# Performance work log

Measured on AMD Instinct MI355X. Metric: run time of the kernel, lower is better.

The kernel has to match this reference:

```python
import jax, jax.numpy as jnp
import numpy as np

# Regularized layout for the per-batch masked attention:
#   batch_size B=8, each batch has NF=2048 'fill' points followed by NK=4096 'keep' points.
B, NF, NK = 8, 2048, 4096
C_IN, C_KQ, C_OUT = 256, 64, 256


def setup_inputs() -> dict:
    key = jax.random.key(0)
    ks = jax.random.split(key, 7)
    N = B * (NF + NK)
    features = jax.random.normal(ks[0], (N, C_IN), dtype=jnp.float32)
    # keep flag: 0 for fill points, 1 for keep points, per batch (fill-first layout)
    flag = jnp.tile(jnp.concatenate([jnp.zeros(NF, jnp.int32), jnp.ones(NK, jnp.int32)]), B)
    s = 1.0 / np.sqrt(C_IN)
    Wq = jax.random.normal(ks[1], (C_KQ, C_IN), jnp.float32) * s
    bq = jnp.zeros((C_KQ,), jnp.float32)
    Wk = jax.random.normal(ks[2], (C_KQ, C_IN), jnp.float32) * s
    bk = jnp.zeros((C_KQ,), jnp.float32)
    Wv = jax.random.normal(ks[3], (C_OUT, C_IN), jnp.float32) * s
    bv = jnp.zeros((C_OUT,), jnp.float32)
    return {"features": features, "keep_flag": flag,
            "Wq": Wq, "bq": bq, "Wk": Wk, "bk": bk, "Wv": Wv, "bv": bv}


def reference(features, keep_flag, Wq, bq, Wk, bk, Wv, bv):
    # features: [N, C_IN]; keep_flag encodes the fill/keep split, which in this
    # regular layout is: first NF rows of each batch are fill, remaining NK are keep.
    del keep_flag  # structure is encoded in the layout (fill-first per batch)
    f = features.reshape(B, NF + NK, C_IN)
    fill = f[:, :NF]             # [B, NF, C_IN]
    keep = f[:, NF:]             # [B, NK, C_IN]
    q = fill @ Wq.T + bq         # [B, NF, C_KQ]
    k = keep @ Wk.T + bk         # [B, NK, C_KQ]
    v = keep @ Wv.T + bv         # [B, NK, C_OUT]
    ratio = np.sqrt(C_KQ).astype(np.float32)
    scores = jnp.einsum('bfd,bkd->bfk', q, k) / ratio   # [B, NF, NK]
    attn = jax.nn.softmax(scores, axis=-1)
    out_fill = jnp.einsum('bfk,bkc->bfc', attn, v)      # [B, NF, C_OUT]
    # keep rows pass through unchanged (only fill rows are overwritten)
    out = jnp.concatenate([out_fill, keep], axis=1)
    return out.reshape(B * (NF + NK), C_OUT)
```

## Files before the change

### kernel.cpp

```cpp
#include <hip/hip_runtime.h>
#include <hip/hip_bf16.h>

#define BATCHES 8
#define NFILL 2048
#define NKEEP 4096
#define SEQLEN 6144
#define CIN 256
#define CKQ 64
#define COUT 256

#define KSC 0.18033688011112042f
#define KOFF -11.541560327111707f

typedef __bf16 bf16_t;
typedef float f32x4 __attribute__((ext_vector_type(4)));
typedef bf16_t bf16x8 __attribute__((ext_vector_type(8)));

__device__ inline void cvt8_store(bf16_t* dst, float4 a, float4 b) {
  bf16x8 v;
  v[0] = (bf16_t)a.x; v[1] = (bf16_t)a.y; v[2] = (bf16_t)a.z; v[3] = (bf16_t)a.w;
  v[4] = (bf16_t)b.x; v[5] = (bf16_t)b.y; v[6] = (bf16_t)b.z; v[7] = (bf16_t)b.w;
  *(bf16x8*)dst = v;
}

__global__ __launch_bounds__(256, 2) void gemm_qkv(
    const float* __restrict__ feat, const float* __restrict__ Wq,
    const float* __restrict__ bq, const float* __restrict__ Wk,
    const float* __restrict__ bk, const float* __restrict__ Wv,
    const float* __restrict__ bv, bf16_t* __restrict__ Qw,
    bf16_t* __restrict__ Kw, bf16_t* __restrict__ Vw,
    float* __restrict__ outp) {
  __shared__ bf16_t Xs[64][264];
  __shared__ bf16_t Ws[64][264];

  const int bid = blockIdx.x;
  const bool isQ = bid >= 512;
  const int mb = isQ ? bid - 512 : bid;

  const int t = threadIdx.x;
  const int lane = t & 63;
  const int wv = t >> 6;
  const int l16 = lane & 15;
  const int quad = lane >> 4;

  const int lr = t >> 2;
  const int koff = (t & 3) << 4;

  const int mrow = mb * 64 + lr;
  const int rpb_shift = isQ ? 11 : 12;
  const int batch = mrow >> rpb_shift;
  const int ridx = mrow & ((1 << rpb_shift) - 1);
  const int row_off = isQ ? 0 : NFILL;
  const long grow = (long)(batch * SEQLEN + row_off + ridx);
  const float* xptr = feat + grow * CIN;
  float4* orow = (float4*)(outp + grow * COUT);

  float4 wr[4][4];
  {
    const float* wrow0 = (isQ ? Wq : Wk) + (long)lr * CIN + koff;
#pragma unroll
    for (int j = 0; j < 4; j++)
#pragma unroll
      for (int s = 0; s < 4; s++)
        wr[j][s] = *(const float4*)(wrow0 + j * 64 + s * 4);
  }

#pragma unroll
  for (int j = 0; j < 4; j++) {
    const int c = koff + j * 64;
    float4 x0 = *(const float4*)(xptr + c);
    float4 x1 = *(const float4*)(xptr + c + 4);
    float4 x2 = *(const float4*)(xptr + c + 8);
    float4 x3 = *(const float4*)(xptr + c + 12);
    cvt8_store(&Xs[lr][c], x0, x1);
    cvt8_store(&Xs[lr][c + 8], x2, x3);
    if (!isQ) {
      orow[(c >> 2) + 0] = x0;
      orow[(c >> 2) + 1] = x1;
      orow[(c >> 2) + 2] = x2;
      orow[(c >> 2) + 3] = x3;
    }
  }
  __syncthreads();

  const int NT = isQ ? 1 : 5;
  const int vb = (mb * 64) >> 12;
  const int key0base = (mb * 64) & 4095;

  for (int nt = 0; nt < NT; nt++) {
#pragma unroll
    for (int j = 0; j < 4; j++) {
      cvt8_store(&Ws[lr][j * 64 + koff], wr[j][0], wr[j][1]);
      cvt8_store(&Ws[lr][j * 64 + koff + 8], wr[j][2], wr[j][3]);
    }
    if (nt + 1 < NT) {
      const float* wrow = Wv + ((long)(nt * 64) + lr) * CIN + koff;
#pragma unroll
      for (int j = 0; j < 4; j++)
#pragma unroll
        for (int s = 0; s < 4; s++)
          wr[j][s] = *(const float4*)(wrow + j * 64 + s * 4);
    }
    asm volatile("s_waitcnt lgkmcnt(0)\n\ts_barrier" ::: "memory");

    f32x4 acc[4];
#pragma unroll
    for (int nb = 0; nb < 4; nb++) acc[nb] = f32x4{0.f, 0.f, 0.f, 0.f};

    if (nt == 0) {
#pragma unroll
      for (int k0 = 0; k0 < CIN; k0 += 64) {
#pragma unroll
        for (int ks = 0; ks < 2; ks++) {
          bf16x8 afrag = *(const bf16x8*)&Xs[wv * 16 + l16][k0 + ks * 32 + quad * 8];
#pragma unroll
          for (int nb = 0; nb < 4; nb++) {
            bf16x8 bfrag = *(const bf16x8*)&Ws[nb * 16 + l16][k0 + ks * 32 + quad * 8];
            acc[nb] = __builtin_amdgcn_mfma_f32_16x16x32_bf16(afrag, bfrag, acc[nb], 0, 0, 0);
          }
        }
      }
      const float* bias = isQ ? bq : bk;
      bf16_t* op = isQ ? Qw : Kw;
#pragma unroll
      for (int nb = 0; nb < 4; nb++) {
        const int n = nb * 16 + l16;
        const float bb = bias[n];
#pragma unroll
        for (int r = 0; r < 4; r++) {
          const int m = mb * 64 + wv * 16 + quad * 4 + r;
          op[(long)m * CKQ + n] = (bf16_t)(acc[nb][r] + bb);
        }
      }
    } else {
#pragma unroll
      for (int k0 = 0; k0 < CIN; k0 += 64) {
#pragma unroll
        for (int ks = 0; ks < 2; ks++) {
          bf16x8 xfrag = *(const bf16x8*)&Xs[wv * 16 + l16][k0 + ks * 32 + quad * 8];
#pragma unroll
          for (int nb = 0; nb < 4; nb++) {
            bf16x8 wfrag = *(const bf16x8*)&Ws[nb * 16 + l16][k0 + ks * 32 + quad * 8];
            acc[nb] = __builtin_amdgcn_mfma_f32_16x16x32_bf16(wfrag, xfrag, acc[nb], 0, 0, 0);
          }
        }
      }
      const int n0 = (nt - 1) * 64;
#pragma unroll
      for (int nb = 0; nb < 4; nb++) {
        f32x4 bbv = *(const f32x4*)&bv[n0 + nb * 16 + quad * 4];
        bf16_t* vdst = Vw +
                       ((long)(vb * COUT + n0 + nb * 16 + quad * 4)) * NKEEP +
                       key0base + wv * 16 + l16;
#pragma unroll
        for (int r = 0; r < 4; r++)
          vdst[(long)r * NKEEP] = (bf16_t)(acc[nb][r] + bbv[r]);
      }
    }

    if (nt + 1 < NT)
      asm volatile("s_waitcnt lgkmcnt(0)\n\ts_barrier" ::: "memory");
  }
}

__global__ __launch_bounds__(256) void attn_kernel(
    const bf16_t* __restrict__ Q, const bf16_t* __restrict__ K,
    const bf16_t* __restrict__ Vt, float* __restrict__ outp) {
  __shared__ bf16_t Ks[2][64][72];
  __shared__ bf16_t Ps[64][72];
  __shared__ float Lsh[64];

  const int qt = blockIdx.x;
  const int b = blockIdx.y;
  const int t = threadIdx.x;
  const int lane = t & 63;
  const int wv = t >> 6;
  const int l16 = lane & 15;
  const int quad = lane >> 4;

  const int krow = t >> 2;
  const int kcol = (t & 3) << 4;

  const bf16_t* kbase = K + (long)b * NKEEP * CKQ;
  const int c0 = wv * 64;
  const bf16_t* vlane =
      Vt + ((long)(b * COUT + c0 + l16)) * NKEEP + quad * 8;

  bf16x8 qfrag[2];
  {
    const bf16_t* qrow = Q + ((long)(b * NFILL + qt * 64 + wv * 16 + l16)) * CKQ;
#pragma unroll
    for (int ks = 0; ks < 2; ks++)
      qfrag[ks] = *(const bf16x8*)(qrow + ks * 32 + quad * 8);
  }

  f32x4 oacc[4][4];
#pragma unroll
  for (int m = 0; m < 4; m++)
#pragma unroll
    for (int ct = 0; ct < 4; ct++) oacc[m][ct] = f32x4{0.f, 0.f, 0.f, 0.f};
  float rsum[4] = {0.f, 0.f, 0.f, 0.f};

  uint4 kreg0, kreg1;
  bf16x8 vA[8], vB[8];

  {
    const bf16_t* ksrc = kbase + (long)krow * CKQ + kcol;
    uint4 k0 = *(const uint4*)ksrc;
    uint4 k1 = *(const uint4*)(ksrc + 8);
#pragma unroll
    for (int ct = 0; ct < 4; ct++)
#pragma unroll
      for (int ks = 0; ks < 2; ks++)
        vA[ct * 2 + ks] = *(const bf16x8*)(vlane + (long)ct * 16 * NKEEP + ks * 32);
    *(uint4*)&Ks[0][krow][kcol] = k0;
    *(uint4*)&Ks[0][krow][kcol + 8] = k1;
  }

#define ATTN_TILE(BUF, VCUR, VNEXT, TV)                                         \
  {                                                                             \
    __syncthreads(); \
    const int tn = ((TV) + 1 < 64) ? (TV) + 1 : 63;                             \
    {                                                                           \
      const bf16_t* ksrc = kbase + ((long)(tn * 64 + krow)) * CKQ + kcol;       \
      kreg0 = *(const uint4*)ksrc;                                              \
      kreg1 = *(const uint4*)(ksrc + 8);                                        \
      const bf16_t* vsrc = vlane + (long)tn * 64;                               \
      _Pragma("unroll") for (int ct = 0; ct < 4; ct++)                          \
          _Pragma("unroll") for (int ks = 0; ks < 2; ks++)                      \
              VNEXT[ct * 2 + ks] =                                              \
          *(const bf16x8*)(vsrc + (long)ct * 16 * NKEEP + ks * 32);             \
    }                                                                           \
    f32x4 sacc[4];                                                              \
    _Pragma("unroll") for (int nb = 0; nb < 4; nb++)                            \
        sacc[nb] = f32x4{0.f, 0.f, 0.f, 0.f};                                   \
    _Pragma("unroll") for (int ks = 0; ks < 2; ks++) {                          \
      _Pragma("unroll") for (int nb = 0; nb < 4; nb++) {                        \
        bf16x8 kfrag = *(const bf16x8*)&Ks[BUF][nb * 16 + l16][ks * 32 + quad * 8]; \
        sacc[nb] = __builtin_amdgcn_mfma_f32_16x16x32_bf16(qfrag[ks], kfrag,    \
                                                           sacc[nb], 0, 0, 0); \
      }                                                                         \
    }                                                                           \
    _Pragma("unroll") for (int nb = 0; nb < 4; nb++) {                          \
      _Pragma("unroll") for (int r = 0; r < 4; r++) {                           \
        const float p = __builtin_exp2f(fmaf(sacc[nb][r], KSC, KOFF));          \
        rsum[r] += p;                                                           \
        Ps[wv * 16 + quad * 4 + r][nb * 16 + l16] = (bf16_t)p;                  \
      }                                                                         \
    }                                                                           \
    asm volatile("s_waitcnt lgkmcnt(0)\n\ts_barrier" ::: "memory");      \
    _Pragma("unroll") for (int ks = 0; ks < 2; ks++) {                          \
      _Pragma("unroll") for (int m = 0; m < 4; m++) {                           \
        bf16x8 pfrag = *(const bf16x8*)&Ps[m * 16 + l16][ks * 32 + quad * 8];   \
        _Pragma("unroll") for (int ct = 0; ct < 4; ct++)                        \
            oacc[m][ct] = __builtin_amdgcn_mfma_f32_16x16x32_bf16(              \
                pfrag, VCUR[ct * 2 + ks], oacc[m][ct], 0, 0, 0);                \
      }                                                                         \
    }                                                                           \
    *(uint4*)&Ks[BUF ^ 1][krow][kcol] = kreg0;                                  \
    *(uint4*)&Ks[BUF ^ 1][krow][kcol + 8] = kreg1;                              \
  }

#pragma unroll 1
  for (int tv = 0; tv < 64; tv += 2) {
    ATTN_TILE(0, vA, vB, tv)
    ATTN_TILE(1, vB, vA, tv + 1)
  }
#undef ATTN_TILE

#pragma unroll
  for (int off = 1; off < 16; off <<= 1)
#pragma unroll
    for (int r = 0; r < 4; r++) rsum[r] += __shfl_xor(rsum[r], off, 64);
  if (l16 == 0) {
#pragma unroll
    for (int r = 0; r < 4; r++) Lsh[wv * 16 + quad * 4 + r] = rsum[r];
  }
  __syncthreads();

  float rl[4][4];
#pragma unroll
  for (int m = 0; m < 4; m++)
#pragma unroll
    for (int r = 0; r < 4; r++) rl[m][r] = 1.0f / Lsh[m * 16 + quad * 4 + r];

  const long obase = ((long)(b * SEQLEN + qt * 64)) * COUT + c0;
#pragma unroll
  for (int m = 0; m < 4; m++)
#pragma unroll
    for (int ct = 0; ct < 4; ct++)
#pragma unroll
      for (int r = 0; r < 4; r++)
        outp[obase + (long)(m * 16 + quad * 4 + r) * COUT + ct * 16 + l16] =
            oacc[m][ct][r] * rl[m][r];
}

extern "C" void kernel_launch(void* const* d_in, const int* in_sizes, int n_in,
                              void* d_out, int out_size, void* d_ws, size_t ws_size,
                              hipStream_t stream) {
  const float* feat = (const float*)d_in[0];
  const float* Wq = (const float*)d_in[2];
  const float* bq = (const float*)d_in[3];
  const float* Wk = (const float*)d_in[4];
  const float* bk = (const float*)d_in[5];
  const float* Wv = (const float*)d_in[6];
  const float* bv = (const float*)d_in[7];
  float* outp = (float*)d_out;

  bf16_t* Qw = (bf16_t*)d_ws;
  bf16_t* Kw = Qw + (size_t)BATCHES * NFILL * CKQ;
  bf16_t* Vw = Kw + (size_t)BATCHES * NKEEP * CKQ;

  gemm_qkv<<<dim3(768), 256, 0, stream>>>(feat, Wq, bq, Wk, bk, Wv, bv,
                                          Qw, Kw, Vw, outp);
  attn_kernel<<<dim3(NFILL / 64, BATCHES), 256, 0, stream>>>(Qw, Kw, Vw, outp);
}
```

Baseline: 204.3 us.

## Double-buffer weight tiles in K-chunks to cut LDS and registers in QKV GEMM

```diff
diff --git a/kernel.cpp b/kernel.cpp
--- a/kernel.cpp
+++ b/kernel.cpp
@@ -23,7 +23,7 @@
   *(bf16x8*)dst = v;
 }
 
-__global__ __launch_bounds__(256, 2) void gemm_qkv(
+__global__ __launch_bounds__(256, 3) void gemm_qkv(
     const float* __restrict__ feat, const float* __restrict__ Wq,
     const float* __restrict__ bq, const float* __restrict__ Wk,
     const float* __restrict__ bk, const float* __restrict__ Wv,
@@ -31,7 +31,7 @@
     bf16_t* __restrict__ Kw, bf16_t* __restrict__ Vw,
     float* __restrict__ outp) {
   __shared__ bf16_t Xs[64][264];
-  __shared__ bf16_t Ws[64][264];
+  __shared__ bf16_t Ws[2][64][72];
 
   const int bid = blockIdx.x;
   const bool isQ = bid >= 512;
@@ -55,14 +55,19 @@
   const float* xptr = feat + grow * CIN;
   float4* orow = (float4*)(outp + grow * COUT);
 
-  float4 wr[4][4];
+  const int NT = isQ ? 1 : 5;
+  const int G = NT * 4;
+  const float* w0src = isQ ? Wq : Wk;
+
+#define WCHUNK_PTR(g)                                                        \
+  (((g) < 4 ? w0src : Wv + (long)((((g) >> 2) - 1) * 64) * CIN) +            \
+   (long)lr * CIN + ((g)&3) * 64 + koff)
+
+  float4 wr[2][4];
   {
-    const float* wrow0 = (isQ ? Wq : Wk) + (long)lr * CIN + koff;
-#pragma unroll
-    for (int j = 0; j < 4; j++)
-#pragma unroll
-      for (int s = 0; s < 4; s++)
-        wr[j][s] = *(const float4*)(wrow0 + j * 64 + s * 4);
+    const float* wp = WCHUNK_PTR(0);
+#pragma unroll
+    for (int s = 0; s < 4; s++) wr[0][s] = *(const float4*)(wp + s * 4);
   }
 
 #pragma unroll
@@ -81,45 +86,69 @@
       orow[(c >> 2) + 3] = x3;
     }
   }
-  __syncthreads();
-
-  const int NT = isQ ? 1 : 5;
+  cvt8_store(&Ws[0][lr][koff], wr[0][0], wr[0][1]);
+  cvt8_store(&Ws[0][lr][koff + 8], wr[0][2], wr[0][3]);
+  {
+    const float* wp = WCHUNK_PTR(1);
+#pragma unroll
+    for (int s = 0; s < 4; s++) wr[1][s] = *(const float4*)(wp + s * 4);
+  }
+  asm volatile("s_waitcnt lgkmcnt(0)\n\ts_barrier" ::: "memory");
+
   const int vb = (mb * 64) >> 12;
   const int key0base = (mb * 64) & 4095;
 
+  f32x4 acc[4];
+#pragma unroll 1
   for (int nt = 0; nt < NT; nt++) {
 #pragma unroll
-    for (int j = 0; j < 4; j++) {
-      cvt8_store(&Ws[lr][j * 64 + koff], wr[j][0], wr[j][1]);
-      cvt8_store(&Ws[lr][j * 64 + koff + 8], wr[j][2], wr[j][3]);
-    }
-    if (nt + 1 < NT) {
-      const float* wrow = Wv + ((long)(nt * 64) + lr) * CIN + koff;
-#pragma unroll
-      for (int j = 0; j < 4; j++)
-#pragma unroll
-        for (int s = 0; s < 4; s++)
-          wr[j][s] = *(const float4*)(wrow + j * 64 + s * 4);
-    }
-    asm volatile("s_waitcnt lgkmcnt(0)\n\ts_barrier" ::: "memory");
-
-    f32x4 acc[4];
-#pragma unroll
     for (int nb = 0; nb < 4; nb++) acc[nb] = f32x4{0.f, 0.f, 0.f, 0.f};
 
-    if (nt == 0) {
-#pragma unroll
-      for (int k0 = 0; k0 < CIN; k0 += 64) {
+#pragma unroll
+    for (int kc = 0; kc < 4; kc++) {
+      const int g = nt * 4 + kc;
+      const int cb = g & 1;
+      const bool last = (g + 1 == G);
+
+      if (!last) {
+        cvt8_store(&Ws[cb ^ 1][lr][koff], wr[cb ^ 1][0], wr[cb ^ 1][1]);
+        cvt8_store(&Ws[cb ^ 1][lr][koff + 8], wr[cb ^ 1][2], wr[cb ^ 1][3]);
+      }
+      if (g + 2 < G) {
+        const float* wp = WCHUNK_PTR(g + 2);
+#pragma unroll
+        for (int s = 0; s < 4; s++) wr[cb][s] = *(const float4*)(wp + s * 4);
+      }
+
+      if (nt == 0) {
 #pragma unroll
         for (int ks = 0; ks < 2; ks++) {
-          bf16x8 afrag = *(const bf16x8*)&Xs[wv * 16 + l16][k0 + ks * 32 + quad * 8];
+          bf16x8 afrag =
+              *(const bf16x8*)&Xs[wv * 16 + l16][kc * 64 + ks * 32 + quad * 8];
 #pragma unroll
           for (int nb = 0; nb < 4; nb++) {
-            bf16x8 bfrag = *(const bf16x8*)&Ws[nb * 16 + l16][k0 + ks * 32 + quad * 8];
+            bf16x8 bfrag = *(const bf16x8*)&Ws[cb][nb * 16 + l16][ks * 32 + quad * 8];
             acc[nb] = __builtin_amdgcn_mfma_f32_16x16x32_bf16(afrag, bfrag, acc[nb], 0, 0, 0);
           }
         }
-      }
+      } else {
+#pragma unroll
+        for (int ks = 0; ks < 2; ks++) {
+          bf16x8 xfrag =
+              *(const bf16x8*)&Xs[wv * 16 + l16][kc * 64 + ks * 32 + quad * 8];
+#pragma unroll
+          for (int nb = 0; nb < 4; nb++) {
+            bf16x8 wfrag = *(const bf16x8*)&Ws[cb][nb * 16 + l16][ks * 32 + quad * 8];
+            acc[nb] = __builtin_amdgcn_mfma_f32_16x16x32_bf16(wfrag, xfrag, acc[nb], 0, 0, 0);
+          }
+        }
+      }
+
+      if (!last)
+        asm volatile("s_waitcnt lgkmcnt(0)\n\ts_barrier" ::: "memory");
+    }
+
+    if (nt == 0) {
       const float* bias = isQ ? bq : bk;
       bf16_t* op = isQ ? Qw : Kw;
 #pragma unroll
@@ -133,18 +162,6 @@
         }
       }
     } else {
-#pragma unroll
-      for (int k0 = 0; k0 < CIN; k0 += 64) {
-#pragma unroll
-        for (int ks = 0; ks < 2; ks++) {
-          bf16x8 xfrag = *(const bf16x8*)&Xs[wv * 16 + l16][k0 + ks * 32 + quad * 8];
-#pragma unroll
-          for (int nb = 0; nb < 4; nb++) {
-            bf16x8 wfrag = *(const bf16x8*)&Ws[nb * 16 + l16][k0 + ks * 32 + quad * 8];
-            acc[nb] = __builtin_amdgcn_mfma_f32_16x16x32_bf16(wfrag, xfrag, acc[nb], 0, 0, 0);
-          }
-        }
-      }
       const int n0 = (nt - 1) * 64;
 #pragma unroll
       for (int nb = 0; nb < 4; nb++) {
@@ -157,10 +174,8 @@
           vdst[(long)r * NKEEP] = (bf16_t)(acc[nb][r] + bbv[r]);
       }
     }
-
-    if (nt + 1 < NT)
-      asm volatile("s_waitcnt lgkmcnt(0)\n\ts_barrier" ::: "memory");
-  }
+  }
+#undef WCHUNK_PTR
 }
 
 __global__ __launch_bounds__(256) void attn_kernel(
```

Result: no change. 205.4 us (+0.5%).
